# Performance work log

Measured on AMD Instinct MI355X. Metric: run time of the kernel, lower is better.

Reference implementation:

```python
import jax, jax.numpy as jnp
import numpy as np
import math

N, M = 50000, 32
ATOM_F = 128
NBR_F = 64
SH_DIM = 9  # (lmax+1)^2 with lmax=2


def setup_inputs() -> dict:
    key = jax.random.key(0)
    k = jax.random.split(key, 8)
    atom_fea = jax.random.normal(k[0], (N, ATOM_F), dtype=jnp.float32)
    nbr_fea = jax.random.normal(k[1], (N, M, NBR_F), dtype=jnp.float32)
    nbr_idx = jax.random.randint(k[2], (N, M), 0, N, dtype=jnp.int64)
    # radial MLP: Linear(NBR_F,NBR_F) -> Softplus -> Linear(NBR_F,SH_DIM)
    w1 = jax.random.normal(k[3], (NBR_F, NBR_F), dtype=jnp.float32) / np.sqrt(NBR_F)
    b1 = jnp.zeros((NBR_F,), dtype=jnp.float32)
    w2 = jax.random.normal(k[4], (NBR_F, SH_DIM), dtype=jnp.float32) / np.sqrt(NBR_F)
    b2 = jnp.zeros((SH_DIM,), dtype=jnp.float32)
    # FullyConnectedTensorProduct(ATOM_Fx0e, 0e+1o+2e, ATOM_Fx0e): the only
    # allowed path is 0e x 0e -> 0e, weight shape [ATOM_F, 1, ATOM_F] -> [ATOM_F, ATOM_F]
    tp_w = jax.random.normal(k[5], (ATOM_F, ATOM_F), dtype=jnp.float32)
    return {"atom_fea": atom_fea, "nbr_fea": nbr_fea, "nbr_idx": nbr_idx,
            "w1": w1, "b1": b1, "w2": w2, "b2": b2, "tp_w": tp_w}


def reference(atom_fea, nbr_fea, nbr_idx, w1, b1, w2, b2, tp_w):
    n, m, _ = nbr_fea.shape
    f = atom_fea.shape[1]
    idx = nbr_idx.reshape(-1)                      # [N*M]
    neigh = atom_fea[idx]                          # [N*M, F] gather
    radial = nbr_fea.reshape(n * m, -1)            # [N*M, NBR_F]
    R = jax.nn.softplus(radial @ w1 + b1) @ w2 + b2  # [N*M, SH_DIM]
    # pos=None path: Y = ones, so W = Y * R = R; only the 0e channel W[:,0]
    # couples in the tensor product. Path normalization: 1/sqrt(mul_in1*mul_in2).
    scalar = R[:, 0]                               # [N*M]
    msg = (neigh @ tp_w) * scalar[:, None] / math.sqrt(f)  # [N*M, F]
    # scatter-mean over neighbor indices (as in source: idx_i = nbr_idx.view(-1))
    sums = jax.ops.segment_sum(msg, idx, num_segments=n)   # [N, F]
    cnt = jax.ops.segment_sum(jnp.ones((n * m,), msg.dtype), idx, num_segments=n)
    out = sums / jnp.maximum(cnt, 1.0)[:, None]
    return out * 1.0  # scale = 1.0 ** 0.5
```

## Files before the change

kernel.cpp:

```cpp
#include <hip/hip_runtime.h>
#include <hip/hip_bf16.h>

#define NATOM 50000
#define MNBR  32
#define NEDGE (NATOM * MNBR)
#define ATOMF 128
#define NBRF  64
#define SHDIM 9
#define NREP_MAX 8

typedef float  f32x4  __attribute__((ext_vector_type(4)));
typedef __bf16 bf16x8 __attribute__((ext_vector_type(8)));

__device__ __forceinline__ float softplus_f(float x) {
    float e = __builtin_amdgcn_exp2f(-fabsf(x) * 1.44269504089f);
    float l = __builtin_amdgcn_logf(1.0f + e);
    return fmaxf(x, 0.0f) + 0.69314718056f * l;
}

__device__ __forceinline__ bf16x8 to_bf16x8(float4 lo, float4 hi) {
    bf16x8 r;
    r[0] = (__bf16)lo.x; r[1] = (__bf16)lo.y; r[2] = (__bf16)lo.z; r[3] = (__bf16)lo.w;
    r[4] = (__bf16)hi.x; r[5] = (__bf16)hi.y; r[6] = (__bf16)hi.z; r[7] = (__bf16)hi.w;
    return r;
}

__global__ __launch_bounds__(256, 4) void edge_kernel(
    const float* __restrict__ nbr_fea, const int* __restrict__ nbr_idx,
    const float* __restrict__ w1, const float* __restrict__ b1,
    const float* __restrict__ w2,
    float* __restrict__ SC, int rep_mask)
{
    const int lane = threadIdx.x & 63;
    const int m    = lane & 15;
    const int quad = lane >> 4;
    const int wave_id = (int)((blockIdx.x * blockDim.x + threadIdx.x) >> 6);
    const int nwaves  = (int)((gridDim.x * blockDim.x) >> 6);

    float* mySC = SC + (size_t)(blockIdx.x & (unsigned)rep_mask) * (2 * NATOM);

    bf16x8 bfrag[2][4];
#pragma unroll
    for (int c = 0; c < 2; ++c)
#pragma unroll
        for (int nb = 0; nb < 4; ++nb)
#pragma unroll
            for (int j = 0; j < 8; ++j)
                bfrag[c][nb][j] = (__bf16)w1[(c * 32 + quad * 8 + j) * NBRF + nb * 16 + m];

    float b1v[4], w2v[4];
#pragma unroll
    for (int nb = 0; nb < 4; ++nb) {
        b1v[nb] = b1[nb * 16 + m];
        w2v[nb] = w2[(nb * 16 + m) * SHDIM + 0];
    }

    const int ntiles = NEDGE / 16;
    int t = wave_id;
    if (t >= ntiles) return;

    float4 pf0, pf1, pf2, pf3;
    int pjj;
    {
        const float* base = &nbr_fea[(size_t)(t * 16 + m) * NBRF + quad * 8];
        pf0 = *(const float4*)(base);
        pf1 = *(const float4*)(base + 4);
        pf2 = *(const float4*)(base + 32);
        pf3 = *(const float4*)(base + 36);
        pjj = nbr_idx[t * 16 + (lane & 15)];
    }

    for (;;) {
        const int e0 = t * 16;
        const int tn = t + nwaves;
        const bool more = (tn < ntiles);

        const bf16x8 af0 = to_bf16x8(pf0, pf1);
        const bf16x8 af1 = to_bf16x8(pf2, pf3);
        int jj = pjj;
        jj = (jj < 0) ? 0 : (jj >= NATOM ? NATOM - 1 : jj);

        if (more) {
            const float* base = &nbr_fea[(size_t)(tn * 16 + m) * NBRF + quad * 8];
            pf0 = *(const float4*)(base);
            pf1 = *(const float4*)(base + 4);
            pf2 = *(const float4*)(base + 32);
            pf3 = *(const float4*)(base + 36);
            pjj = nbr_idx[tn * 16 + (lane & 15)];
        }

        f32x4 acc[4] = { {0.f,0.f,0.f,0.f}, {0.f,0.f,0.f,0.f},
                         {0.f,0.f,0.f,0.f}, {0.f,0.f,0.f,0.f} };
#pragma unroll
        for (int nb = 0; nb < 4; ++nb) {
            acc[nb] = __builtin_amdgcn_mfma_f32_16x16x32_bf16(af0, bfrag[0][nb], acc[nb], 0, 0, 0);
            acc[nb] = __builtin_amdgcn_mfma_f32_16x16x32_bf16(af1, bfrag[1][nb], acc[nb], 0, 0, 0);
        }

        float part[4] = {0.f, 0.f, 0.f, 0.f};
#pragma unroll
        for (int nb = 0; nb < 4; ++nb)
#pragma unroll
            for (int r = 0; r < 4; ++r)
                part[r] += softplus_f(acc[nb][r] + b1v[nb]) * w2v[nb];

#pragma unroll
        for (int off = 1; off < 16; off <<= 1)
#pragma unroll
            for (int r = 0; r < 4; ++r)
                part[r] += __shfl_xor(part[r], off, 64);

        const int src = ((lane & 15) >> 2) << 4;
        const float t0 = __shfl(part[0], src, 64);
        const float t1 = __shfl(part[1], src, 64);
        const float t2 = __shfl(part[2], src, 64);
        const float t3 = __shfl(part[3], src, 64);
        const int rr = lane & 3;
        const float val = (rr == 0) ? t0 : (rr == 1) ? t1 : (rr == 2) ? t2 : t3;

        if (lane < 16) {
            atomicAdd(&mySC[2 * jj],     val);
            atomicAdd(&mySC[2 * jj + 1], 1.0f);
        }

        if (!more) break;
        t = tn;
    }
}

__global__ __launch_bounds__(256) void atom_kernel(
    const float* __restrict__ atom_fea, const float* __restrict__ tp_w,
    const float* __restrict__ SC, const float* __restrict__ b2,
    float* __restrict__ out, int nrep)
{
    const int lane = threadIdx.x & 63;
    const int wave = threadIdx.x >> 6;
    const int m    = lane & 15;
    const int quad = lane >> 4;
    const float b2_0 = b2[0];

    bf16x8 bfrag[4][2];
#pragma unroll
    for (int c = 0; c < 4; ++c)
#pragma unroll
        for (int nb = 0; nb < 2; ++nb)
#pragma unroll
            for (int j = 0; j < 8; ++j)
                bfrag[c][nb][j] =
                    (__bf16)tp_w[(c * 32 + quad * 8 + j) * ATOMF + (wave * 2 + nb) * 16 + m];

    const int p     = m & 7;
    const int which = m >> 3;

    const int ntiles = NATOM / 16;
    for (int t = blockIdx.x; t < ntiles; t += gridDim.x) {
        const int j0 = t * 16;

        bf16x8 afrag[4];
#pragma unroll
        for (int c = 0; c < 4; ++c) {
            const float* base = &atom_fea[(size_t)(j0 + m) * ATOMF + c * 32 + quad * 8];
            const float4 f0 = *(const float4*)(base);
            const float4 f1 = *(const float4*)(base + 4);
            afrag[c] = to_bf16x8(f0, f1);
        }

        f32x4 acc[2] = { {0.f,0.f,0.f,0.f}, {0.f,0.f,0.f,0.f} };
#pragma unroll
        for (int c = 0; c < 4; ++c)
#pragma unroll
            for (int nb = 0; nb < 2; ++nb)
                acc[nb] = __builtin_amdgcn_mfma_f32_16x16x32_bf16(
                    afrag[c], bfrag[c][nb], acc[nb], 0, 0, 0);

        float scv[4];
#pragma unroll
        for (int r = 0; r < 4; ++r) {
            const int j = j0 + quad * 4 + r;
            float v = (p < nrep) ? SC[(size_t)p * (2 * NATOM) + 2 * j + which] : 0.f;
#pragma unroll
            for (int off = 1; off < 8; off <<= 1)
                v += __shfl_xor(v, off, 64);
            const float o = __shfl_xor(v, 8, 64);
            const float s = which ? o : v;
            const float c = which ? v : o;
            scv[r] = (s + c * b2_0) / fmaxf(c, 1.0f) * 0.08838834764831843f;
        }

#pragma unroll
        for (int nb = 0; nb < 2; ++nb)
#pragma unroll
            for (int r = 0; r < 4; ++r)
                out[(size_t)(j0 + quad * 4 + r) * ATOMF + (wave * 2 + nb) * 16 + m] =
                    acc[nb][r] * scv[r];
    }
}

extern "C" void kernel_launch(void* const* d_in, const int* in_sizes, int n_in,
                              void* d_out, int out_size, void* d_ws, size_t ws_size,
                              hipStream_t stream) {
    const float* atom_fea = (const float*)d_in[0];
    const float* nbr_fea  = (const float*)d_in[1];
    const int*   nbr_idx  = (const int*)d_in[2];
    const float* w1       = (const float*)d_in[3];
    const float* b1       = (const float*)d_in[4];
    const float* w2       = (const float*)d_in[5];
    const float* b2       = (const float*)d_in[6];
    const float* tp_w     = (const float*)d_in[7];
    float* out = (float*)d_out;

    float* SC = (float*)d_ws;

    int nrep = (ws_size >= (size_t)NREP_MAX * 2 * NATOM * sizeof(float)) ? NREP_MAX : 1;

    hipMemsetAsync(d_ws, 0, (size_t)nrep * 2 * NATOM * sizeof(float), stream);

    edge_kernel<<<2048, 256, 0, stream>>>(nbr_fea, nbr_idx, w1, b1, w2, SC, nrep - 1);
    atom_kernel<<<1024, 256, 0, stream>>>(atom_fea, tp_w, SC, b2, out, nrep);
}
```

Measured before the change: 622.1 us.

## Pack per-atom sum and count into a single double atomic

Encodes each edge contribution as a double holding the scalar plus a large fixed offset (2^32), so one 64-bit atomic add updates both the sum and the neighbor count. This halves the number of scatter atomics and removes the shuffle-gather to lane 0..15, letting four lanes per quad issue atomics directly. The atom kernel decodes the count by rounding and recovers the sum by subtraction. The trade-off is 64-bit atomics and reduced precision of the sum relative to the large count offset.

```diff
diff --git a/kernel.cpp b/kernel.cpp
--- a/kernel.cpp
+++ b/kernel.cpp
@@ -8,6 +8,7 @@
 #define NBRF  64
 #define SHDIM 9
 #define NREP_MAX 8
+#define CNT_SCALE 4294967296.0
 
 typedef float  f32x4  __attribute__((ext_vector_type(4)));
 typedef __bf16 bf16x8 __attribute__((ext_vector_type(8)));
@@ -29,7 +30,7 @@
     const float* __restrict__ nbr_fea, const int* __restrict__ nbr_idx,
     const float* __restrict__ w1, const float* __restrict__ b1,
     const float* __restrict__ w2,
-    float* __restrict__ SC, int rep_mask)
+    double* __restrict__ SC, int rep_mask)
 {
     const int lane = threadIdx.x & 63;
     const int m    = lane & 15;
@@ -37,7 +38,7 @@
     const int wave_id = (int)((blockIdx.x * blockDim.x + threadIdx.x) >> 6);
     const int nwaves  = (int)((gridDim.x * blockDim.x) >> 6);
 
-    float* mySC = SC + (size_t)(blockIdx.x & (unsigned)rep_mask) * (2 * NATOM);
+    double* mySC = SC + (size_t)(blockIdx.x & (unsigned)rep_mask) * NATOM;
 
     bf16x8 bfrag[2][4];
 #pragma unroll
@@ -71,14 +72,13 @@
     }
 
     for (;;) {
-        const int e0 = t * 16;
         const int tn = t + nwaves;
         const bool more = (tn < ntiles);
 
         const bf16x8 af0 = to_bf16x8(pf0, pf1);
         const bf16x8 af1 = to_bf16x8(pf2, pf3);
-        int jj = pjj;
-        jj = (jj < 0) ? 0 : (jj >= NATOM ? NATOM - 1 : jj);
+        int jc = pjj;
+        jc = (jc < 0) ? 0 : (jc >= NATOM ? NATOM - 1 : jc);
 
         if (more) {
             const float* base = &nbr_fea[(size_t)(tn * 16 + m) * NBRF + quad * 8];
@@ -110,18 +110,13 @@
             for (int r = 0; r < 4; ++r)
                 part[r] += __shfl_xor(part[r], off, 64);
 
-        const int src = ((lane & 15) >> 2) << 4;
-        const float t0 = __shfl(part[0], src, 64);
-        const float t1 = __shfl(part[1], src, 64);
-        const float t2 = __shfl(part[2], src, 64);
-        const float t3 = __shfl(part[3], src, 64);
-        const int rr = lane & 3;
-        const float val = (rr == 0) ? t0 : (rr == 1) ? t1 : (rr == 2) ? t2 : t3;
-
-        if (lane < 16) {
-            atomicAdd(&mySC[2 * jj],     val);
-            atomicAdd(&mySC[2 * jj + 1], 1.0f);
-        }
+        const int rr  = m & 3;
+        const float val = (rr == 0) ? part[0] : (rr == 1) ? part[1]
+                         : (rr == 2) ? part[2] : part[3];
+        const int jje = __shfl(jc, (quad << 2) | rr, 64);
+
+        if (m < 4)
+            unsafeAtomicAdd(&mySC[jje], (double)val + CNT_SCALE);
 
         if (!more) break;
         t = tn;
@@ -130,7 +125,7 @@
 
 __global__ __launch_bounds__(256) void atom_kernel(
     const float* __restrict__ atom_fea, const float* __restrict__ tp_w,
-    const float* __restrict__ SC, const float* __restrict__ b2,
+    const double* __restrict__ SC, const float* __restrict__ b2,
     float* __restrict__ out, int nrep)
 {
     const int lane = threadIdx.x & 63;
@@ -149,8 +144,7 @@
                 bfrag[c][nb][j] =
                     (__bf16)tp_w[(c * 32 + quad * 8 + j) * ATOMF + (wave * 2 + nb) * 16 + m];
 
-    const int p     = m & 7;
-    const int which = m >> 3;
+    const int p = m & 7;
 
     const int ntiles = NATOM / 16;
     for (int t = blockIdx.x; t < ntiles; t += gridDim.x) {
@@ -177,14 +171,15 @@
 #pragma unroll
         for (int r = 0; r < 4; ++r) {
             const int j = j0 + quad * 4 + r;
-            float v = (p < nrep) ? SC[(size_t)p * (2 * NATOM) + 2 * j + which] : 0.f;
+            double v = (m < 8 && p < nrep) ? SC[(size_t)p * NATOM + j] : 0.0;
 #pragma unroll
             for (int off = 1; off < 8; off <<= 1)
                 v += __shfl_xor(v, off, 64);
-            const float o = __shfl_xor(v, 8, 64);
-            const float s = which ? o : v;
-            const float c = which ? v : o;
-            scv[r] = (s + c * b2_0) / fmaxf(c, 1.0f) * 0.08838834764831843f;
+            v += __shfl_xor(v, 8, 64);
+            const double cnt_d = __builtin_rint(v * (1.0 / CNT_SCALE));
+            const float  cf    = (float)cnt_d;
+            const float  sf    = (float)(v - cnt_d * CNT_SCALE);
+            scv[r] = (sf + cf * b2_0) / fmaxf(cf, 1.0f) * 0.08838834764831843f;
         }
 
 #pragma unroll
@@ -209,11 +204,11 @@
     const float* tp_w     = (const float*)d_in[7];
     float* out = (float*)d_out;
 
-    float* SC = (float*)d_ws;
-
-    int nrep = (ws_size >= (size_t)NREP_MAX * 2 * NATOM * sizeof(float)) ? NREP_MAX : 1;
-
-    hipMemsetAsync(d_ws, 0, (size_t)nrep * 2 * NATOM * sizeof(float), stream);
+    double* SC = (double*)d_ws;
+
+    int nrep = (ws_size >= (size_t)NREP_MAX * NATOM * sizeof(double)) ? NREP_MAX : 1;
+
+    hipMemsetAsync(d_ws, 0, (size_t)nrep * NATOM * sizeof(double), stream);
 
     edge_kernel<<<2048, 256, 0, stream>>>(nbr_fea, nbr_idx, w1, b1, w2, SC, nrep - 1);
     atom_kernel<<<1024, 256, 0, stream>>>(atom_fea, tp_w, SC, b2, out, nrep);
```

After: 583.4 us. 6.2% less time.
